# Kernel optimization log

Hardware: AMD Instinct MI355X
Metric: run time of the kernel (lower is better)

The kernel has to match this reference:

```python
import jax, jax.numpy as jnp
import numpy as np

B, T, H, L = 64, 256, 512, 3
CELL_IN = [H + H, H + H + H, H + H]  # layer0: x+top, layer1: x+bottom+top, layer2: x+bottom


def setup_inputs() -> dict:
    key = jax.random.key(0)
    ks = jax.random.split(key, 4 + 4 * L)
    inp = {}
    for l in range(L):
        inp[f"x{l}"] = jax.random.normal(ks[l], (B, T, H), dtype=jnp.float32)
    # boundary indicators in {0,1}
    inp["dx"] = jax.random.bernoulli(ks[3], 0.3, (B, L, T)).astype(jnp.float32)
    s = 1.0 / np.sqrt(H)  # torch LSTMCell default init range
    k = 4
    for l in range(L):
        inp[f"W_ih{l}"] = jax.random.uniform(ks[k], (4 * H, CELL_IN[l]), jnp.float32, -s, s); k += 1
        inp[f"W_hh{l}"] = jax.random.uniform(ks[k], (4 * H, H), jnp.float32, -s, s); k += 1
        inp[f"b_ih{l}"] = jax.random.uniform(ks[k], (4 * H,), jnp.float32, -s, s); k += 1
        inp[f"b_hh{l}"] = jax.random.uniform(ks[k], (4 * H,), jnp.float32, -s, s); k += 1
    return inp


def _hmlstm(xs, dx, params):
    # xs: list of L arrays [B,T,H]; dx: [B,L,T]
    dx_t = jnp.transpose(dx, (2, 0, 1))                                 # [T,B,L] : d at time t
    dx_prev = jnp.concatenate([jnp.zeros_like(dx_t[:1]), dx_t[:-1]], 0)  # d at t-1 (zeros at t=0)
    xs_t = tuple(jnp.transpose(x, (1, 0, 2)) for x in xs)               # [T,B,H]
    h0 = tuple(jnp.zeros((B, H), jnp.float32) for _ in range(L))
    c0 = tuple(jnp.zeros((B, H), jnp.float32) for _ in range(L))

    def step(carry, inputs):
        h_prev, c_prev = carry
        x0t, x1t, x2t, dt, dpt = inputs
        x_t = [x0t, x1t, x2t]
        h_new, c_new = [], []
        for l in range(L):
            W_ih, W_hh, b_ih, b_hh = params[l]
            d_bottom = jnp.ones((B, 1), jnp.float32) if l == 0 else dt[:, l - 1:l]
            d = dpt[:, l:l + 1]
            xin = x_t[l] * d_bottom
            if l > 0:
                xin = jnp.concatenate([xin, h_new[l - 1] * d_bottom], axis=-1)  # bottom-up, same timestep
            if l < L - 1:
                xin = jnp.concatenate([xin, h_prev[l + 1] * d], axis=-1)        # top-down, previous timestep
            h = h_prev[l]
            c = c_prev[l] * (1.0 - d)  # flush cell on boundary
            gates = xin @ W_ih.T + h @ W_hh.T + b_ih + b_hh
            i, f, g, o = jnp.split(gates, 4, axis=-1)  # torch LSTMCell gate order
            i = jax.nn.sigmoid(i); f = jax.nn.sigmoid(f)
            g = jnp.tanh(g); o = jax.nn.sigmoid(o)
            c_ = f * c + i * g
            h_ = o * jnp.tanh(c_)
            copy = ((d_bottom + d) == 0.0).astype(jnp.float32)  # COPY op: keep old state
            h_new.append(copy * h + (1.0 - copy) * h_)
            c_new.append(copy * c + (1.0 - copy) * c_)
        carry = (tuple(h_new), tuple(c_new))
        return carry, tuple(h_new)

    _, hs = jax.lax.scan(step, (h0, c0), (xs_t[0], xs_t[1], xs_t[2], dx_t, dx_prev))
    return tuple(jnp.transpose(h, (1, 0, 2)) for h in hs)  # L x [B,T,H]


def reference(x0, x1, x2, dx,
              W_ih0, W_hh0, b_ih0, b_hh0,
              W_ih1, W_hh1, b_ih1, b_hh1,
              W_ih2, W_hh2, b_ih2, b_hh2):
    params = [(W_ih0, W_hh0, b_ih0, b_hh0),
              (W_ih1, W_hh1, b_ih1, b_hh1),
              (W_ih2, W_hh2, b_ih2, b_hh2)]
    return _hmlstm([x0, x1, x2], dx, params)
```

## Files before the change

kernel.cpp:

```cpp
#include <hip/hip_runtime.h>
#include <math.h>

#define BB 64
#define TT 256
#define HH 512
#define TH (TT*HH)
#define BTH (BB*TT*HH)

typedef __attribute__((ext_vector_type(8))) short short8;
typedef __attribute__((ext_vector_type(4))) float f32x4;

__device__ __forceinline__ unsigned short f32_bf16(float f) {
    unsigned int u = __float_as_uint(f);
    return (unsigned short)((u + 0x7fffu + ((u >> 16) & 1u)) >> 16);
}

__device__ __forceinline__ float sigm_f(float x) {
    return 1.f / (1.f + __expf(-x));
}
__device__ __forceinline__ float tanh_f(float x) {
    return 1.f - 2.f / (__expf(2.f * x) + 1.f);
}

__device__ __forceinline__ short8 ld_coh(const short* p) {
    const unsigned long long* q = (const unsigned long long*)p;
    unsigned long long a = __hip_atomic_load(q,     __ATOMIC_RELAXED, __HIP_MEMORY_SCOPE_AGENT);
    unsigned long long b = __hip_atomic_load(q + 1, __ATOMIC_RELAXED, __HIP_MEMORY_SCOPE_AGENT);
    union { unsigned long long u[2]; short8 s; } r;
    r.u[0] = a; r.u[1] = b;
    return r.s;
}

struct WConv2 {
    const float* src[3][4];
    int rs[3][4];
    int co[3][4];
    int nch[3];
    int cnt[3];
    unsigned int slab[3];
    short* dst;
};
__global__ __launch_bounds__(256) void conv_w(WConv2 a) {
    const int l = blockIdx.y;
    const int i = blockIdx.x * 256 + threadIdx.x;
    if (i >= a.cnt[l]) return;
    const int NCH = a.nch[l];
    const int lane = i & 63;
    const int r = i >> 6;
    const int scc = r % NCH;
    const int wv = r / NCH;
    const int kh = wv & 1;
    const int nt = (wv >> 1) & 3;
    const int nb = wv >> 3;
    const int seg = scc >> 3;
    const int cc = scc & 7;
    const int hcol = nb*16 + nt*4 + ((lane & 15) >> 2);
    const int q = lane & 3;
    const int row = q*512 + hcol;
    const int k = a.co[l][seg] + (cc*2 + kh)*32 + (lane >> 4)*8;
    const float* s = a.src[l][seg] + (size_t)row * a.rs[l][seg] + k;
    float4 v0 = *(const float4*)s;
    float4 v1 = *(const float4*)(s + 4);
    short8 o;
    o[0]=f32_bf16(v0.x); o[1]=f32_bf16(v0.y); o[2]=f32_bf16(v0.z); o[3]=f32_bf16(v0.w);
    o[4]=f32_bf16(v1.x); o[5]=f32_bf16(v1.y); o[6]=f32_bf16(v1.z); o[7]=f32_bf16(v1.w);
    *(short8*)(a.dst + (size_t)a.slab[l] + (size_t)i * 8) = o;
}

struct XConv {
    const float* src[3];
    short* dst;
};
__global__ __launch_bounds__(256) void conv_x(XConv a) {
    const int l = blockIdx.y;
    const int i = blockIdx.x * 256 + threadIdx.x;
    const int lane = i & 63;
    const int kc = (i >> 6) & 15;
    const int btt = i >> 10;
    const int bt = btt & 3;
    const int t = btt >> 2;
    const int b = bt * 16 + (lane & 15);
    const int k = kc * 32 + (lane >> 4) * 8;
    const float* s = a.src[l] + ((size_t)b * TT + t) * HH + k;
    float4 v0 = *(const float4*)s;
    float4 v1 = *(const float4*)(s + 4);
    short8 o;
    o[0]=f32_bf16(v0.x); o[1]=f32_bf16(v0.y); o[2]=f32_bf16(v0.z); o[3]=f32_bf16(v0.w);
    o[4]=f32_bf16(v1.x); o[5]=f32_bf16(v1.y); o[6]=f32_bf16(v1.z); o[7]=f32_bf16(v1.w);
    *(short8*)(a.dst + (size_t)l * 8388608 + (size_t)i * 8) = o;
}

struct PersArgs {
    const short* wreg; const short* xreg; short* hreg;
    const float* dx; float* out; int* flags;
    const float* bih[3]; const float* bhh[3];
};

#define SEG_MFMA_PLAIN(SB, ASRC, SCP)                                          \
    {                                                                          \
        const short* ap_ = (ASRC) + (size_t)lane * 8;                          \
        _Pragma("unroll")                                                      \
        for (int cc = 0; cc < 8; ++cc) {                                       \
            const int cis = cc*2 + kh;                                         \
            short8 av[4];                                                      \
            _Pragma("unroll")                                                  \
            for (int mt = 0; mt < 4; ++mt)                                     \
                av[mt] = *(const short8*)(ap_ + (size_t)(mt*16 + cis) * 512);  \
            _Pragma("unroll")                                                  \
            for (int mt = 0; mt < 4; ++mt) {                                   \
                short8 xa = ((SCP) == nullptr || (SCP)[mt] != 0.f) ? av[mt] : vz; \
                acc[mt] = __builtin_amdgcn_mfma_f32_16x16x32_bf16(             \
                    xa, w[(SB) + cc], acc[mt], 0, 0, 0);                       \
            }                                                                  \
        }                                                                      \
    }

#define SEG_LDSMM_H(SB, ABUF, SCP, MT0)                                        \
    _Pragma("unroll")                                                          \
    for (int cc = 0; cc < 8; ++cc) {                                           \
        _Pragma("unroll")                                                      \
        for (int m2 = 0; m2 < 2; ++m2) {                                       \
            short8 av = *(const short8*)((ABUF) + (size_t)(m2*16 + cc*2 + kh)*512 + lane*8); \
            short8 xa = ((SCP) == nullptr || (SCP)[(MT0)+m2] != 0.f) ? av : vz; \
            acc[(MT0)+m2] = __builtin_amdgcn_mfma_f32_16x16x32_bf16(           \
                xa, w[(SB) + cc], acc[(MT0)+m2], 0, 0, 0);                     \
        }                                                                      \
    }

#define SEG_COH_LDS(SB, ASRC, SCP)                                             \
    {                                                                          \
        const short* spA_ = (ASRC) + ((size_t)(wv*4))*512 + lane*8;            \
        const short* spB_ = (ASRC) + ((size_t)(32 + wv*4))*512 + lane*8;       \
        short8 a0_ = ld_coh(spA_);                                             \
        short8 a1_ = ld_coh(spA_ + 512);                                       \
        short8 a2_ = ld_coh(spA_ + 1024);                                      \
        short8 a3_ = ld_coh(spA_ + 1536);                                      \
        short8 b0_ = ld_coh(spB_);                                             \
        short8 b1_ = ld_coh(spB_ + 512);                                       \
        short8 b2_ = ld_coh(spB_ + 1024);                                      \
        short8 b3_ = ld_coh(spB_ + 1536);                                      \
        {                                                                      \
            short* dp_ = abufA + (wv*4)*512 + lane*8;                          \
            *(short8*)(dp_)        = a0_;                                      \
            *(short8*)(dp_ + 512)  = a1_;                                      \
            *(short8*)(dp_ + 1024) = a2_;                                      \
            *(short8*)(dp_ + 1536) = a3_;                                      \
        }                                                                      \
        asm volatile("s_waitcnt lgkmcnt(0)" ::: "memory");                     \
        __builtin_amdgcn_s_barrier();                                          \
        __builtin_amdgcn_sched_barrier(0);                                     \
        SEG_LDSMM_H(SB, abufA, SCP, 0);                                        \
        {                                                                      \
            short* dpB_ = abufB + (wv*4)*512 + lane*8;                         \
            *(short8*)(dpB_)        = b0_;                                     \
            *(short8*)(dpB_ + 512)  = b1_;                                     \
            *(short8*)(dpB_ + 1024) = b2_;                                     \
            *(short8*)(dpB_ + 1536) = b3_;                                     \
        }                                                                      \
        __syncthreads();                                                       \
        SEG_LDSMM_H(SB, abufB, SCP, 2);                                        \
    }

template<int L>
__device__ __forceinline__ void run_layer(const PersArgs& a, int nb,
                                          char* smem) {
    constexpr int NSEG = (L == 1) ? 4 : 3;
    constexpr int NCH  = NSEG * 8;
    constexpr unsigned int WSLAB = (L == 0) ? 0u : ((L == 1) ? 3145728u : 7340032u);
    short* abufA = (short*)smem;
    short* abufB = (short*)(smem + 32768);
    float* gsh   = (float*)smem;
    #define GSH(khi, nti, mti, ri, ci) gsh[((((khi)*4 + (nti))*4 + (mti))*16 + (ri))*16 + (ci)]

    const int tid  = threadIdx.x;
    const int lane = tid & 63;
    const int wv   = tid >> 6;
    const int nt   = wv >> 1;
    const int kh   = wv & 1;
    const int r16  = lane & 15;
    const short8 vz = {0,0,0,0,0,0,0,0};

    short8 w[NCH];
    {
        const short* wb = a.wreg + WSLAB
            + ((size_t)((nb*8 + nt*2 + kh) * NCH)) * 512 + lane * 8;
        #pragma unroll
        for (int i = 0; i < NCH; ++i)
            w[i] = *(const short8*)(wb + (size_t)i * 512);
    }

    const int eb_b = tid >> 3;
    const int ehp  = tid & 7;
    float bias[2][4];
    #pragma unroll
    for (int e = 0; e < 2; ++e) {
        const int ec = nb*16 + 2*ehp + e;
        #pragma unroll
        for (int q = 0; q < 4; ++q)
            bias[e][q] = a.bih[L][q*512 + ec] + a.bhh[L][q*512 + ec];
    }
    float c_reg[2] = {0.f, 0.f}, h_reg[2] = {0.f, 0.f};
    float hprev[2] = {0.f, 0.f};

    auto poll32 = [&](int st) {
        if (wv == 0) {
            const int* f = a.flags + st*32;
            for (;;) {
                int v = 1;
                if (lane < 32)
                    v = __hip_atomic_load(f + lane, __ATOMIC_RELAXED, __HIP_MEMORY_SCOPE_AGENT);
                if (__all(v != 0)) break;
                __builtin_amdgcn_s_sleep(1);
            }
        }
        __syncthreads();
    };

    for (int t = 0; t < TT; ++t) {
        const int pprev = (t - 1) & 1, pcur = t & 1;
        float dbv[4], dvv[4];
        #pragma unroll
        for (int mt = 0; mt < 4; ++mt) {
            const int b = mt*16 + r16;
            dbv[mt] = (L == 0) ? 1.f : a.dx[b*768 + (L-1)*256 + t];
            dvv[mt] = (t == 0) ? 0.f : a.dx[b*768 + L*256 + (t-1)];
        }
        f32x4 acc[4];
        #pragma unroll
        for (int mt = 0; mt < 4; ++mt) acc[mt] = (f32x4){0.f, 0.f, 0.f, 0.f};

        SEG_MFMA_PLAIN(0, a.xreg + (size_t)L*8388608 + (size_t)t*32768,
                       (L == 0) ? (const float*)nullptr : dbv);

        if (t > 0) {
            poll32((t-1)*3 + L);
            {
                union { float f[2]; unsigned long long u; } pk;
                pk.f[0] = hprev[0]; pk.f[1] = hprev[1];
                __builtin_nontemporal_store(pk.u,
                    (unsigned long long*)(a.out + (size_t)L*BTH + (size_t)eb_b*TH
                                          + (size_t)(t-1)*HH + nb*16 + 2*ehp));
            }
            SEG_COH_LDS(8, a.hreg + (size_t)(L*2 + pprev)*32768, (const float*)nullptr);
            if (L < 2) {
                poll32((t-1)*3 + L + 1);
                SEG_COH_LDS(16, a.hreg + (size_t)((L+1)*2 + pprev)*32768, dvv);
            }
        }
        if (L > 0) {
            poll32(t*3 + L - 1);
            SEG_COH_LDS(NCH - 8, a.hreg + (size_t)((L-1)*2 + pcur)*32768, dbv);
        }

        #pragma unroll
        for (int mt = 0; mt < 4; ++mt)
            #pragma unroll
            for (int r = 0; r < 4; ++r)
                GSH(kh, nt, mt, (lane >> 4)*4 + r, r16) = acc[mt][r];
        __syncthreads();

        float hval[2];
        {
            const float db2 = (L == 0) ? 1.f : a.dx[eb_b*768 + (L-1)*256 + t];
            const float d2  = (t == 0) ? 0.f : a.dx[eb_b*768 + L*256 + (t-1)];
            const bool copy = (db2 + d2 == 0.f);
            const int mt = eb_b >> 4, row = eb_b & 15;
            #pragma unroll
            for (int e = 0; e < 2; ++e) {
                const int hl = 2*ehp + e;
                const int ntE = hl >> 2, cb = (hl & 3)*4;
                float G[4];
                #pragma unroll
                for (int q = 0; q < 4; ++q)
                    G[q] = GSH(0, ntE, mt, row, cb+q) + GSH(1, ntE, mt, row, cb+q) + bias[e][q];
                const float i_ = sigm_f(G[0]);
                const float f_ = sigm_f(G[1]);
                const float g_ = tanh_f(G[2]);
                const float o_ = sigm_f(G[3]);
                const float cold = c_reg[e] * (1.f - d2);
                const float cn = f_*cold + i_*g_;
                const float hn = o_*tanh_f(cn);
                hval[e] = copy ? h_reg[e] : hn;
                c_reg[e] = copy ? cold : cn;
                h_reg[e] = hval[e];
            }
            unsigned int pack = (unsigned int)f32_bf16(hval[0])
                              | ((unsigned int)f32_bf16(hval[1]) << 16);
            const int k  = nb*16 + 2*ehp;
            const int kc = k >> 5, kk = k & 31;
            const int lhi = kk >> 3, j = kk & 7;
            unsigned int* dst = (unsigned int*)(a.hreg + (size_t)(L*2 + pcur)*32768)
                + ((((size_t)(mt*16 + kc))*64 + lhi*16 + row)*8 + j) / 2;
            __hip_atomic_store(dst, pack, __ATOMIC_RELAXED, __HIP_MEMORY_SCOPE_AGENT);
        }
        __syncthreads();

        if (tid == 0)
            __hip_atomic_store(a.flags + (t*3 + L)*32 + nb, 1,
                               __ATOMIC_RELAXED, __HIP_MEMORY_SCOPE_AGENT);

        hprev[0] = hval[0]; hprev[1] = hval[1];
    }
    {
        union { float f[2]; unsigned long long u; } pk;
        pk.f[0] = hprev[0]; pk.f[1] = hprev[1];
        __builtin_nontemporal_store(pk.u,
            (unsigned long long*)(a.out + (size_t)L*BTH + (size_t)eb_b*TH
                                  + (size_t)(TT-1)*HH + nb*16 + 2*ehp));
    }
    #undef GSH
}

__global__ __launch_bounds__(512, 2) void persistent_kernel(PersArgs a) {
    __shared__ char smem[65536];
    const int bid = blockIdx.x;
    if (bid < 32)       run_layer<0>(a, bid, smem);
    else if (bid < 64)  run_layer<1>(a, bid - 32, smem);
    else                run_layer<2>(a, bid - 64, smem);
}

extern "C" void kernel_launch(void* const* d_in, const int* in_sizes, int n_in,
                              void* d_out, int out_size, void* d_ws, size_t ws_size,
                              hipStream_t stream) {
    const float* x[3]    = {(const float*)d_in[0], (const float*)d_in[1], (const float*)d_in[2]};
    const float* dx      = (const float*)d_in[3];
    const float* W_ih[3] = {(const float*)d_in[4], (const float*)d_in[8],  (const float*)d_in[12]};
    const float* W_hh[3] = {(const float*)d_in[5], (const float*)d_in[9],  (const float*)d_in[13]};
    const float* b_ih[3] = {(const float*)d_in[6], (const float*)d_in[10], (const float*)d_in[14]};
    const float* b_hh[3] = {(const float*)d_in[7], (const float*)d_in[11], (const float*)d_in[15]};
    float* out = (float*)d_out;

    char* ws = (char*)d_ws;
    const size_t SZ_FLAGS = 98304;
    const size_t SZ_WREG  = 20971520;
    const size_t SZ_XREG  = 50331648;
    int*   flags = (int*)ws;
    short* wreg  = (short*)(ws + SZ_FLAGS);
    short* xreg  = (short*)(ws + SZ_FLAGS + SZ_WREG);
    short* hreg  = (short*)(ws + SZ_FLAGS + SZ_WREG + SZ_XREG);

    hipMemsetAsync(flags, 0, SZ_FLAGS, stream);

    {
        WConv2 wa;
        wa.src[0][0]=W_ih[0]; wa.rs[0][0]=1024; wa.co[0][0]=0;
        wa.src[0][1]=W_hh[0]; wa.rs[0][1]=512;  wa.co[0][1]=0;
        wa.src[0][2]=W_ih[0]; wa.rs[0][2]=1024; wa.co[0][2]=512;
        wa.src[0][3]=W_ih[0]; wa.rs[0][3]=1024; wa.co[0][3]=0;
        wa.src[1][0]=W_ih[1]; wa.rs[1][0]=1536; wa.co[1][0]=0;
        wa.src[1][1]=W_hh[1]; wa.rs[1][1]=512;  wa.co[1][1]=0;
        wa.src[1][2]=W_ih[1]; wa.rs[1][2]=1536; wa.co[1][2]=1024;
        wa.src[1][3]=W_ih[1]; wa.rs[1][3]=1536; wa.co[1][3]=512;
        wa.src[2][0]=W_ih[2]; wa.rs[2][0]=1024; wa.co[2][0]=0;
        wa.src[2][1]=W_hh[2]; wa.rs[2][1]=512;  wa.co[2][1]=0;
        wa.src[2][2]=W_ih[2]; wa.rs[2][2]=1024; wa.co[2][2]=512;
        wa.src[2][3]=W_ih[2]; wa.rs[2][3]=1024; wa.co[2][3]=0;
        wa.nch[0]=24; wa.nch[1]=32; wa.nch[2]=24;
        wa.cnt[0]=393216; wa.cnt[1]=524288; wa.cnt[2]=393216;
        wa.slab[0]=0; wa.slab[1]=3145728; wa.slab[2]=7340032;
        wa.dst = wreg;
        conv_w<<<dim3(2048, 3), 256, 0, stream>>>(wa);
    }
    {
        XConv xa;
        xa.src[0] = x[0]; xa.src[1] = x[1]; xa.src[2] = x[2];
        xa.dst = xreg;
        conv_x<<<dim3(4096, 3), 256, 0, stream>>>(xa);
    }

    PersArgs pa;
    pa.wreg = wreg; pa.xreg = xreg; pa.hreg = hreg;
    pa.dx = dx; pa.out = out; pa.flags = flags;
    for (int l = 0; l < 3; ++l) { pa.bih[l] = b_ih[l]; pa.bhh[l] = b_hh[l]; }
    persistent_kernel<<<dim3(96), 512, 0, stream>>>(pa);
}
```

Measured before the change: 3.296 ms.

## Use per-wave completion flags instead of block barrier before signaling

Each of the 8 waves in a block now publishes its own flag after its h stores drain, so the block-wide barrier before the flag store is gone. Consumers poll 256 flags per step with two 64-bit atomic loads per lane instead of 32. The barrier after the LDS gate writes becomes a raw s_barrier with an explicit lgkmcnt wait. The aim is to cut barrier latency on the serial per-timestep critical path, at the cost of more flag memory and wider polling. Dropping the trailing barrier may let a wave start the next timestep's LDS writes while other waves are still reading gates from LDS.

```diff
diff --git a/kernel.cpp b/kernel.cpp
--- a/kernel.cpp
+++ b/kernel.cpp
@@ -202,14 +202,16 @@
     float c_reg[2] = {0.f, 0.f}, h_reg[2] = {0.f, 0.f};
     float hprev[2] = {0.f, 0.f};
 
-    auto poll32 = [&](int st) {
+    auto poll256 = [&](int st) {
         if (wv == 0) {
-            const int* f = a.flags + st*32;
+            const unsigned long long* f =
+                (const unsigned long long*)(a.flags + st*256) + lane*2;
             for (;;) {
-                int v = 1;
-                if (lane < 32)
-                    v = __hip_atomic_load(f + lane, __ATOMIC_RELAXED, __HIP_MEMORY_SCOPE_AGENT);
-                if (__all(v != 0)) break;
+                unsigned long long v0 = __hip_atomic_load(f,     __ATOMIC_RELAXED, __HIP_MEMORY_SCOPE_AGENT);
+                unsigned long long v1 = __hip_atomic_load(f + 1, __ATOMIC_RELAXED, __HIP_MEMORY_SCOPE_AGENT);
+                const bool ok = ((unsigned int)v0 != 0u) && ((v0 >> 32) != 0u)
+                             && ((unsigned int)v1 != 0u) && ((v1 >> 32) != 0u);
+                if (__all(ok)) break;
                 __builtin_amdgcn_s_sleep(1);
             }
         }
@@ -233,7 +235,7 @@
                        (L == 0) ? (const float*)nullptr : dbv);
 
         if (t > 0) {
-            poll32((t-1)*3 + L);
+            poll256((t-1)*3 + L);
             {
                 union { float f[2]; unsigned long long u; } pk;
                 pk.f[0] = hprev[0]; pk.f[1] = hprev[1];
@@ -243,12 +245,12 @@
             }
             SEG_COH_LDS(8, a.hreg + (size_t)(L*2 + pprev)*32768, (const float*)nullptr);
             if (L < 2) {
-                poll32((t-1)*3 + L + 1);
+                poll256((t-1)*3 + L + 1);
                 SEG_COH_LDS(16, a.hreg + (size_t)((L+1)*2 + pprev)*32768, dvv);
             }
         }
         if (L > 0) {
-            poll32(t*3 + L - 1);
+            poll256(t*3 + L - 1);
             SEG_COH_LDS(NCH - 8, a.hreg + (size_t)((L-1)*2 + pcur)*32768, dbv);
         }
 
@@ -257,7 +259,9 @@
             #pragma unroll
             for (int r = 0; r < 4; ++r)
                 GSH(kh, nt, mt, (lane >> 4)*4 + r, r16) = acc[mt][r];
-        __syncthreads();
+        asm volatile("s_waitcnt lgkmcnt(0)" ::: "memory");
+        __builtin_amdgcn_s_barrier();
+        __builtin_amdgcn_sched_barrier(0);
 
         float hval[2];
         {
@@ -293,10 +297,10 @@
                 + ((((size_t)(mt*16 + kc))*64 + lhi*16 + row)*8 + j) / 2;
             __hip_atomic_store(dst, pack, __ATOMIC_RELAXED, __HIP_MEMORY_SCOPE_AGENT);
         }
-        __syncthreads();
-
-        if (tid == 0)
-            __hip_atomic_store(a.flags + (t*3 + L)*32 + nb, 1,
+
+        asm volatile("s_waitcnt vmcnt(0)" ::: "memory");
+        if (lane == 0)
+            __hip_atomic_store(a.flags + (t*3 + L)*256 + nb*8 + wv, 1,
                                __ATOMIC_RELAXED, __HIP_MEMORY_SCOPE_AGENT);
 
         hprev[0] = hval[0]; hprev[1] = hval[1];
@@ -331,7 +335,7 @@
     float* out = (float*)d_out;
 
     char* ws = (char*)d_ws;
-    const size_t SZ_FLAGS = 98304;
+    const size_t SZ_FLAGS = 786432;
     const size_t SZ_WREG  = 20971520;
     const size_t SZ_XREG  = 50331648;
     int*   flags = (int*)ws;
```

New measurement: 3.464 ms. +5.1%, slower.
